# Kernel optimization log

Hardware: AMD Instinct MI355X
Metric: run time of the kernel (lower is better)

The kernel has to match this reference:

```python
import jax, jax.numpy as jnp
import numpy as np
import math

L, B, T, S, E, H, F = 6, 8, 1024, 1024, 1024, 16, 4096
HD = E // H
EPS = 1e-5

def setup_inputs() -> dict:
    key = jax.random.key(0)
    ks = jax.random.split(key, 20)
    def n(k, shape, s=0.02):
        return jax.random.normal(k, shape, dtype=jnp.float32) * s
    return {
        'encoder_output': n(ks[0], (B, S, E), 1.0),
        'decoder_input': n(ks[1], (B, T, E), 1.0),
        # LayerNorm params (stacked over layers)
        'ln1_w': jnp.ones((L, E), jnp.float32), 'ln1_b': jnp.zeros((L, E), jnp.float32),
        'ln2_w': jnp.ones((L, E), jnp.float32), 'ln2_b': jnp.zeros((L, E), jnp.float32),
        'ln3_w': jnp.ones((L, E), jnp.float32), 'ln3_b': jnp.zeros((L, E), jnp.float32),
        # self-attention: per-head wq/wk/wv concatenated into [E,E] (x @ W convention)
        'Wq_s': n(ks[2], (L, E, E)), 'Wk_s': n(ks[3], (L, E, E)), 'Wv_s': n(ks[4], (L, E, E)),
        'Wo_s': n(ks[5], (L, E, E)), 'bo_s': jnp.zeros((L, E), jnp.float32),
        # cross-attention
        'Wq_c': n(ks[6], (L, E, E)), 'Wk_c': n(ks[7], (L, E, E)), 'Wv_c': n(ks[8], (L, E, E)),
        'Wo_c': n(ks[9], (L, E, E)), 'bo_c': jnp.zeros((L, E), jnp.float32),
        # FFN
        'W1': n(ks[10], (L, E, F)), 'b1': jnp.zeros((L, F), jnp.float32),
        'W2': n(ks[11], (L, F, E)), 'b2': jnp.zeros((L, E), jnp.float32),
    }

def _layernorm(x, w, b):
    m = jnp.mean(x, axis=-1, keepdims=True)
    v = jnp.mean(jnp.square(x - m), axis=-1, keepdims=True)
    return (x - m) * jax.lax.rsqrt(v + EPS) * w + b

def _split_heads(x):
    b, s, _ = x.shape
    return x.reshape(b, s, H, HD).transpose(0, 2, 1, 3)  # [B,H,S,HD]

def _mha(q_in, k_in, v_in, Wq, Wk, Wv, Wo, bo, mask):
    q = _split_heads(q_in @ Wq)
    k = _split_heads(k_in @ Wk)
    v = _split_heads(v_in @ Wv)
    scores = jnp.einsum('bhqd,bhkd->bhqk', q, k) / math.sqrt(HD)
    if mask is not None:
        scores = jnp.where(mask, scores, jnp.float32(-jnp.inf))
    attn = jax.nn.softmax(scores, axis=-1)
    out = jnp.einsum('bhqk,bhkd->bhqd', attn, v)
    out = out.transpose(0, 2, 1, 3).reshape(q_in.shape[0], q_in.shape[1], E)
    return out @ Wo + bo

def reference(encoder_output, decoder_input,
              ln1_w, ln1_b, ln2_w, ln2_b, ln3_w, ln3_b,
              Wq_s, Wk_s, Wv_s, Wo_s, bo_s,
              Wq_c, Wk_c, Wv_c, Wo_c, bo_c,
              W1, b1, W2, b2):
    causal = jnp.tril(jnp.ones((T, T), dtype=bool))  # [T,T] -> broadcast over B,H
    params = (ln1_w, ln1_b, ln2_w, ln2_b, ln3_w, ln3_b,
              Wq_s, Wk_s, Wv_s, Wo_s, bo_s,
              Wq_c, Wk_c, Wv_c, Wo_c, bo_c,
              W1, b1, W2, b2)

    def layer(x, p):
        (l1w, l1b, l2w, l2b, l3w, l3b,
         wqs, wks, wvs, wos, bos,
         wqc, wkc, wvc, woc, boc,
         w1, bb1, w2, bb2) = p
        nx = _layernorm(x, l1w, l1b)
        x = x + _mha(nx, nx, nx, wqs, wks, wvs, wos, bos, causal)
        x = x + _mha(_layernorm(x, l2w, l2b), encoder_output, encoder_output,
                     wqc, wkc, wvc, woc, boc, None)
        h = _layernorm(x, l3w, l3b)
        x = x + (jax.nn.gelu(h @ w1 + bb1) @ w2 + bb2)
        return x, None

    out, _ = jax.lax.scan(layer, decoder_input, params)
    return out
```

## Files before the change

### kernel.cpp

```cpp
#include <hip/hip_runtime.h>
#include <cstdint>

typedef __bf16 bf16;
typedef __bf16 bf16x8 __attribute__((ext_vector_type(8)));
typedef __bf16 bf16x4 __attribute__((ext_vector_type(4)));
typedef float f32x4 __attribute__((ext_vector_type(4)));

static_assert(sizeof(bf16) == 2, "bf16 size");

constexpr int LAYERS = 6;
constexpr int BATCH  = 8;
constexpr int TDEC   = 1024;
constexpr int SENC   = 1024;
constexpr int EMB    = 1024;
constexpr int NH     = 16;
constexpr int FFN    = 4096;
constexpr int MTOK   = BATCH * TDEC;

typedef __attribute__((address_space(1))) void gvoid;
typedef __attribute__((address_space(3))) void lvoid;

__device__ __forceinline__ void gload16(const void* g, void* l) {
  __builtin_amdgcn_global_load_lds((gvoid*)(uintptr_t)g,
                                   (lvoid*)(uint32_t)(uintptr_t)l,
                                   16, 0, 0);
}

__device__ __forceinline__ f32x4 mfma_16x16x32(bf16x8 a, bf16x8 b, f32x4 c) {
  return __builtin_amdgcn_mfma_f32_16x16x32_bf16(a, b, c, 0, 0, 0);
}

__global__ void k_cvt(const float* __restrict__ in, bf16* __restrict__ outp, int n4) {
  int i = blockIdx.x * 256 + threadIdx.x;
  if (i < n4) {
    float4 v = ((const float4*)in)[i];
    bf16x4 o;
    o[0] = (bf16)v.x; o[1] = (bf16)v.y; o[2] = (bf16)v.z; o[3] = (bf16)v.w;
    ((bf16x4*)outp)[i] = o;
  }
}

__launch_bounds__(256)
__global__ void k_transpose(const float* __restrict__ in, bf16* __restrict__ outp,
                            int R, int C) {
  __shared__ float tile[32][33];
  const int tx = threadIdx.x, ty = threadIdx.y;
  const int r0 = blockIdx.y * 32, c0 = blockIdx.x * 32;
#pragma unroll
  for (int i = 0; i < 32; i += 8)
    tile[ty + i][tx] = in[(size_t)(r0 + ty + i) * C + c0 + tx];
  __syncthreads();
#pragma unroll
  for (int i = 0; i < 32; i += 8)
    outp[(size_t)(c0 + ty + i) * R + r0 + tx] = (bf16)tile[tx][ty + i];
}

__launch_bounds__(256)
__global__ void k_transpose4(const float* __restrict__ s0, const float* __restrict__ s1,
                             const float* __restrict__ s2, const float* __restrict__ s3,
                             bf16* __restrict__ d0, bf16* __restrict__ d1,
                             bf16* __restrict__ d2, bf16* __restrict__ d3,
                             int R, int C) {
  const int z = blockIdx.z;
  const float* in = (z == 0) ? s0 : (z == 1) ? s1 : (z == 2) ? s2 : s3;
  bf16* outp      = (z == 0) ? d0 : (z == 1) ? d1 : (z == 2) ? d2 : d3;
  __shared__ float tile[32][33];
  const int tx = threadIdx.x, ty = threadIdx.y;
  const int r0 = blockIdx.y * 32, c0 = blockIdx.x * 32;
#pragma unroll
  for (int i = 0; i < 32; i += 8)
    tile[ty + i][tx] = in[(size_t)(r0 + ty + i) * C + c0 + tx];
  __syncthreads();
#pragma unroll
  for (int i = 0; i < 32; i += 8)
    outp[(size_t)(c0 + ty + i) * R + r0 + tx] = (bf16)tile[tx][ty + i];
}

__launch_bounds__(256)
__global__ void k_layernorm(const float* __restrict__ x, const float* __restrict__ w,
                            const float* __restrict__ bb, bf16* __restrict__ outp) {
  const int row = blockIdx.x;
  const int t = threadIdx.x;
  const float4 v = ((const float4*)(x + (size_t)row * EMB))[t];
  float s = v.x + v.y + v.z + v.w;
  __shared__ float red[4];
#pragma unroll
  for (int off = 32; off > 0; off >>= 1) s += __shfl_down(s, off, 64);
  if ((t & 63) == 0) red[t >> 6] = s;
  __syncthreads();
  const float mean = (red[0] + red[1] + red[2] + red[3]) * (1.0f / EMB);
  const float dx = v.x - mean, dy = v.y - mean, dz = v.z - mean, dw = v.w - mean;
  float ss = dx * dx + dy * dy + dz * dz + dw * dw;
  __syncthreads();
#pragma unroll
  for (int off = 32; off > 0; off >>= 1) ss += __shfl_down(ss, off, 64);
  if ((t & 63) == 0) red[t >> 6] = ss;
  __syncthreads();
  const float var = (red[0] + red[1] + red[2] + red[3]) * (1.0f / EMB);
  const float rstd = rsqrtf(var + 1e-5f);
  const float4 wv = ((const float4*)w)[t];
  const float4 bv = ((const float4*)bb)[t];
  bf16x4 o;
  o[0] = (bf16)(dx * rstd * wv.x + bv.x);
  o[1] = (bf16)(dy * rstd * wv.y + bv.y);
  o[2] = (bf16)(dz * rstd * wv.z + bv.z);
  o[3] = (bf16)(dw * rstd * wv.w + bv.w);
  *(bf16x4*)(outp + (size_t)row * EMB + t * 4) = o;
}

template <int EPI>
__launch_bounds__(256)
__global__ void k_gemm(const bf16* __restrict__ A, const bf16* __restrict__ Bt,
                       int M, int N, int K, int ldc,
                       bf16* __restrict__ outb, float* __restrict__ outf,
                       const float* __restrict__ res, const float* __restrict__ bias) {
  __shared__ __align__(16) bf16 sA[128 * 32];
  __shared__ __align__(16) bf16 sB[128 * 32];
  const int tid = threadIdx.x;
  const int wave = tid >> 6, lane = tid & 63;
  const int quad = lane >> 4, l16 = lane & 15;
  const int wm = wave >> 1, wn = wave & 1;

  int bid = blockIdx.y * gridDim.x + blockIdx.x;
  const int nwg = gridDim.x * gridDim.y;
  if ((nwg & 7) == 0) {
    const int q = nwg >> 3;
    bid = (bid & 7) * q + (bid >> 3);
  }
  const int bn = bid % gridDim.x;
  const int bm = bid / gridDim.x;

  f32x4 acc[4][4] = {};

  const int srow = wave * 16 + (lane >> 2);
  const int scol = (lane & 3) * 8;
  const bf16* Ag = A  + (size_t)(bm * 128 + srow) * K + scol;
  const bf16* Bg = Bt + (size_t)(bn * 128 + srow) * K + scol;
  bf16* sA0 = &sA[(wave * 16) * 32];
  bf16* sA1 = &sA[(wave * 16 + 64) * 32];
  bf16* sB0 = &sB[(wave * 16) * 32];
  bf16* sB1 = &sB[(wave * 16 + 64) * 32];

  const int nk = K >> 5;
  for (int kt = 0; kt < nk; ++kt) {
    gload16(Ag, sA0);
    gload16(Ag + (size_t)64 * K, sA1);
    gload16(Bg, sB0);
    gload16(Bg + (size_t)64 * K, sB1);
    Ag += 32; Bg += 32;
    __syncthreads();
    bf16x8 af[4], bfv[4];
    const bf16* pa = &sA[(wm * 64 + l16) * 32 + quad * 8];
    const bf16* pb = &sB[(wn * 64 + l16) * 32 + quad * 8];
#pragma unroll
    for (int i = 0; i < 4; ++i) af[i] = *(const bf16x8*)(pa + i * 16 * 32);
#pragma unroll
    for (int i = 0; i < 4; ++i) bfv[i] = *(const bf16x8*)(pb + i * 16 * 32);
#pragma unroll
    for (int i = 0; i < 4; ++i)
#pragma unroll
      for (int j = 0; j < 4; ++j)
        acc[i][j] = mfma_16x16x32(af[i], bfv[j], acc[i][j]);
    __syncthreads();
  }

  const int row0 = bm * 128 + wm * 64;
  const int col0 = bn * 128 + wn * 64;
#pragma unroll
  for (int j = 0; j < 4; ++j) {
    const int c = col0 + j * 16 + l16;
    const float bv = (EPI >= 1) ? bias[c] : 0.0f;
#pragma unroll
    for (int i = 0; i < 4; ++i) {
#pragma unroll
      for (int r = 0; r < 4; ++r) {
        const size_t rr = (size_t)(row0 + i * 16 + quad * 4 + r);
        float v = acc[i][j][r];
        if (EPI == 0) {
          outb[rr * ldc + c] = (bf16)v;
        } else if (EPI == 1) {
          v += bv;
          const float u = 0.7978845608028654f * (v + 0.044715f * v * v * v);
          const float g = v / (1.0f + exp2f(u * -2.8853900817779268f));
          outb[rr * ldc + c] = (bf16)g;
        } else {
          outf[rr * ldc + c] = res[rr * ldc + c] + v + bv;
        }
      }
    }
  }
}

template <bool CAUSAL>
__launch_bounds__(256)
__global__ void k_attn(const bf16* __restrict__ Q, const bf16* __restrict__ Kg,
                       const bf16* __restrict__ Vg, bf16* __restrict__ Og,
                       int TQ, int TK, int ld) {
  __shared__ __align__(16) bf16 sK[2][64 * 64];
  __shared__ __align__(16) bf16 sVt[2][64 * 72];
  __shared__ __align__(16) bf16 sP[4][32 * 72];
  const int tid = threadIdx.x;
  const int wave = tid >> 6, lane = tid & 63;
  const int quad = lane >> 4, l16 = lane & 15;

  int bx = blockIdx.x, by = blockIdx.y;
  {
    const int nwg = gridDim.x * gridDim.y;
    if ((nwg & 7) == 0 && (gridDim.y & 7) == 0) {
      const int d = by * gridDim.x + bx;
      const int xcd = d & 7, idx = d >> 3;
      const int hpx = gridDim.y >> 3;
      by = xcd * hpx + idx / gridDim.x;
      bx = idx % gridDim.x;
    }
  }
  const int b = by >> 4;
  const int h = by & 15;
  const int qt = CAUSAL ? (gridDim.x - 1 - bx) : bx;
  const int q0 = qt * 128;
  const int qw = q0 + wave * 32;

  const bf16* Qbase = Q + (size_t)(b * TQ) * ld + h * 64;
  const bf16* Kbase = Kg + (size_t)(b * TK) * ld + h * 64;
  const bf16* Vbase = Vg + (size_t)(b * TK) * ld + h * 64;

  bf16x8 aq[2][2];
#pragma unroll
  for (int m = 0; m < 2; ++m) {
    const bf16* qp = Qbase + (size_t)(qw + m * 16 + l16) * ld + quad * 8;
    aq[m][0] = *(const bf16x8*)(qp);
    aq[m][1] = *(const bf16x8*)(qp + 32);
  }

  bf16x8 vones;
#pragma unroll
  for (int e = 0; e < 8; ++e) vones[e] = (bf16)1.0f;

  f32x4 oacc[2][4] = {};
  float m_[2][4], l_[2][4];
#pragma unroll
  for (int m = 0; m < 2; ++m)
#pragma unroll
    for (int r = 0; r < 4; ++r) { m_[m][r] = -1e30f; l_[m][r] = 0.0f; }

  const int srow = lane >> 3;
  const int schunk = lane & 7;
  bf16* sPw = &sP[wave][0];

  const float sc = 0.125f * 1.44269504088896f;
  const int nj = CAUSAL ? (q0 >> 6) + 2 : (TK >> 6);

#pragma unroll
  for (int r2 = 0; r2 < 2; ++r2) {
    const int rowt = (wave + 4 * r2) * 8 + srow;
    const int gchunk = schunk ^ (rowt & 7);
    gload16(Kbase + (size_t)rowt * ld + gchunk * 8,
            &sK[0][(wave + 4 * r2) * 8 * 64]);
  }
#pragma unroll
  for (int r2 = 0; r2 < 2; ++r2) {
    const int cv = wave + 4 * r2;
    const bf16x8 vv = *(const bf16x8*)(Vbase + (size_t)lane * ld + cv * 8);
#pragma unroll
    for (int e = 0; e < 8; ++e) sVt[0][(cv * 8 + e) * 72 + lane] = vv[e];
  }
  __syncthreads();

  int cur = 0;
  for (int j = 0; j < nj; ++j) {
    const int nxt = cur ^ 1;
    const int k0 = j * 64;
    const bool pre = (j + 1 < nj);
    bf16x8 vpre[2];
    if (pre) {
      const int k0n = k0 + 64;
#pragma unroll
      for (int r2 = 0; r2 < 2; ++r2) {
        const int rowt = (wave + 4 * r2) * 8 + srow;
        const int gchunk = schunk ^ (rowt & 7);
        gload16(Kbase + (size_t)(k0n + rowt) * ld + gchunk * 8,
                &sK[nxt][(wave + 4 * r2) * 8 * 64]);
      }
#pragma unroll
      for (int r2 = 0; r2 < 2; ++r2)
        vpre[r2] = *(const bf16x8*)(Vbase + (size_t)(k0n + lane) * ld +
                                    (wave + 4 * r2) * 8);
    }

    const bool active = !CAUSAL || (k0 <= qw + 31);
    if (active) {
#pragma unroll
      for (int m = 0; m < 2; ++m) {
        f32x4 s[4];
#pragma unroll
        for (int kt = 0; kt < 4; ++kt) {
          const int krow = kt * 16 + l16;
          const int p0 = (quad ^ (l16 & 7)) * 8;
          const int p1 = ((quad + 4) ^ (l16 & 7)) * 8;
          const bf16x8 bk0 = *(const bf16x8*)(&sK[cur][krow * 64 + p0]);
          const bf16x8 bk1 = *(const bf16x8*)(&sK[cur][krow * 64 + p1]);
          f32x4 z = {};
          z = mfma_16x16x32(aq[m][0], bk0, z);
          z = mfma_16x16x32(aq[m][1], bk1, z);
          s[kt] = z;
        }
        const int row_base = qw + m * 16;
        float rowmax[4] = {-1e30f, -1e30f, -1e30f, -1e30f};
        if (CAUSAL && (k0 + 63 > row_base)) {
#pragma unroll
          for (int kt = 0; kt < 4; ++kt) {
            const int key = k0 + kt * 16 + l16;
#pragma unroll
            for (int r = 0; r < 4; ++r) {
              if (key > row_base + quad * 4 + r) s[kt][r] = -1e30f;
              rowmax[r] = fmaxf(rowmax[r], s[kt][r]);
            }
          }
        } else {
#pragma unroll
          for (int kt = 0; kt < 4; ++kt)
#pragma unroll
            for (int r = 0; r < 4; ++r)
              rowmax[r] = fmaxf(rowmax[r], s[kt][r]);
        }
#pragma unroll
        for (int off = 1; off < 16; off <<= 1)
#pragma unroll
          for (int r = 0; r < 4; ++r)
            rowmax[r] = fmaxf(rowmax[r], __shfl_xor(rowmax[r], off, 64));
        float alpha[4], nms[4];
#pragma unroll
        for (int r = 0; r < 4; ++r) {
          const float mn = fmaxf(m_[m][r], rowmax[r]);
          alpha[r] = exp2f((m_[m][r] - mn) * sc);
          m_[m][r] = mn;
          nms[r] = -mn * sc;
        }
#pragma unroll
        for (int kt = 0; kt < 4; ++kt)
#pragma unroll
          for (int r = 0; r < 4; ++r) {
            const float pv = exp2f(fmaf(s[kt][r], sc, nms[r]));
            sPw[(m * 16 + quad * 4 + r) * 72 + kt * 16 + l16] = (bf16)pv;
          }
        const bf16x8 ap0 = *(const bf16x8*)(&sPw[(m * 16 + l16) * 72 + quad * 8]);
        const bf16x8 ap1 = *(const bf16x8*)(&sPw[(m * 16 + l16) * 72 + 32 + quad * 8]);
        f32x4 zs = {};
        zs = mfma_16x16x32(ap0, vones, zs);
        zs = mfma_16x16x32(ap1, vones, zs);
#pragma unroll
        for (int r = 0; r < 4; ++r) {
          l_[m][r] = l_[m][r] * alpha[r] + zs[r];
#pragma unroll
          for (int dt = 0; dt < 4; ++dt) oacc[m][dt][r] *= alpha[r];
        }
#pragma unroll
        for (int dt = 0; dt < 4; ++dt) {
          const bf16x8 bv0 = *(const bf16x8*)(&sVt[cur][(dt * 16 + l16) * 72 + quad * 8]);
          const bf16x8 bv1 = *(const bf16x8*)(&sVt[cur][(dt * 16 + l16) * 72 + 32 + quad * 8]);
          oacc[m][dt] = mfma_16x16x32(ap0, bv0, oacc[m][dt]);
          oacc[m][dt] = mfma_16x16x32(ap1, bv1, oacc[m][dt]);
        }
      }
    }

    if (pre) {
#pragma unroll
      for (int r2 = 0; r2 < 2; ++r2) {
        const int cv = wave + 4 * r2;
#pragma unroll
        for (int e = 0; e < 8; ++e) sVt[nxt][(cv * 8 + e) * 72 + lane] = vpre[r2][e];
      }
    }
    __syncthreads();
    cur = nxt;
  }

#pragma unroll
  for (int m = 0; m < 2; ++m)
#pragma unroll
    for (int r = 0; r < 4; ++r) {
      const float inv = 1.0f / l_[m][r];
      bf16* op = Og + (size_t)(b * TQ + qw + m * 16 + quad * 4 + r) * EMB + h * 64;
#pragma unroll
      for (int dt = 0; dt < 4; ++dt)
        op[dt * 16 + l16] = (bf16)(oacc[m][dt][r] * inv);
    }
}

extern "C" void kernel_launch(void* const* d_in, const int* in_sizes, int n_in,
                              void* d_out, int out_size, void* d_ws, size_t ws_size,
                              hipStream_t stream) {
  const float* enc  = (const float*)d_in[0];
  const float* dec  = (const float*)d_in[1];
  const float* ln1w = (const float*)d_in[2];
  const float* ln1b = (const float*)d_in[3];
  const float* ln2w = (const float*)d_in[4];
  const float* ln2b = (const float*)d_in[5];
  const float* ln3w = (const float*)d_in[6];
  const float* ln3b = (const float*)d_in[7];
  const float* Wq_s = (const float*)d_in[8];
  const float* Wk_s = (const float*)d_in[9];
  const float* Wv_s = (const float*)d_in[10];
  const float* Wo_s = (const float*)d_in[11];
  const float* bo_s = (const float*)d_in[12];
  const float* Wq_c = (const float*)d_in[13];
  const float* Wk_c = (const float*)d_in[14];
  const float* Wv_c = (const float*)d_in[15];
  const float* Wo_c = (const float*)d_in[16];
  const float* bo_c = (const float*)d_in[17];
  const float* W1   = (const float*)d_in[18];
  const float* b1   = (const float*)d_in[19];
  const float* W2   = (const float*)d_in[20];
  const float* b2   = (const float*)d_in[21];
  float* out = (float*)d_out;

  char* p = (char*)d_ws;
  auto take = [&](size_t bytes) {
    char* r = p;
    p += (bytes + 255) & ~(size_t)255;
    return (void*)r;
  };
  bf16* wqkvT = (bf16*)take((size_t)3 * EMB * EMB * 2);
  bf16* woT   = (bf16*)take((size_t)EMB * EMB * 2);
  bf16* w1T   = (bf16*)take((size_t)EMB * FFN * 2);
  bf16* w2T   = (bf16*)take((size_t)FFN * EMB * 2);
  bf16* encb  = (bf16*)take((size_t)BATCH * SENC * EMB * 2);
  float* xbuf = (float*)take((size_t)MTOK * EMB * 4);
  bf16* nx    = (bf16*)take((size_t)MTOK * EMB * 2);
  bf16* qkvb  = (bf16*)take((size_t)MTOK * 3 * EMB * 2);
  bf16* ab    = (bf16*)take((size_t)MTOK * EMB * 2);
  bf16* hb    = (bf16*)take((size_t)MTOK * FFN * 2);
  if ((size_t)((char*)p - (char*)d_ws) > ws_size) return;

  const int LD3 = 3 * EMB;

  {
    const int n4 = BATCH * SENC * EMB / 4;
    k_cvt<<<(n4 + 255) / 256, 256, 0, stream>>>(enc, encb, n4);
  }
  hipMemcpyAsync(xbuf, dec, (size_t)MTOK * EMB * 4, hipMemcpyDeviceToDevice, stream);

  auto trans = [&](const float* w, bf16* wt, int R, int C) {
    k_transpose<<<dim3(C / 32, R / 32), dim3(32, 8), 0, stream>>>(w, wt, R, C);
  };
  auto trans4 = [&](const float* s0, const float* s1, const float* s2, const float* s3,
                    bf16* d0, bf16* d1, bf16* d2, bf16* d3) {
    k_transpose4<<<dim3(EMB / 32, EMB / 32, 4), dim3(32, 8), 0, stream>>>(
        s0, s1, s2, s3, d0, d1, d2, d3, EMB, EMB);
  };
  auto gemm0 = [&](const bf16* Ap, const bf16* Btp, bf16* op, int M, int N, int K,
                   int ldc) {
    k_gemm<0><<<dim3(N / 128, M / 128), 256, 0, stream>>>(Ap, Btp, M, N, K, ldc, op,
                                                          nullptr, nullptr, nullptr);
  };
  auto gemm_gelu = [&](const bf16* Ap, const bf16* Btp, bf16* op, const float* bi,
                       int M, int N, int K) {
    k_gemm<1><<<dim3(N / 128, M / 128), 256, 0, stream>>>(Ap, Btp, M, N, K, N, op,
                                                          nullptr, nullptr, bi);
  };
  auto gemm_res = [&](const bf16* Ap, const bf16* Btp, float* op, const float* rs,
                      const float* bi, int M, int N, int K) {
    k_gemm<2><<<dim3(N / 128, M / 128), 256, 0, stream>>>(Ap, Btp, M, N, K, N, nullptr,
                                                          op, rs, bi);
  };

  for (int l = 0; l < LAYERS; ++l) {
    const size_t wofs = (size_t)l * EMB * EMB;
    k_layernorm<<<MTOK, 256, 0, stream>>>(xbuf, ln1w + l * EMB, ln1b + l * EMB, nx);
    trans4(Wq_s + wofs, Wk_s + wofs, Wv_s + wofs, Wo_s + wofs,
           wqkvT, wqkvT + (size_t)EMB * EMB, wqkvT + (size_t)2 * EMB * EMB, woT);
    gemm0(nx, wqkvT, qkvb, MTOK, 3 * EMB, EMB, LD3);
    k_attn<true><<<dim3(TDEC / 128, BATCH * NH), 256, 0, stream>>>(
        qkvb, qkvb + EMB, qkvb + 2 * EMB, ab, TDEC, TDEC, LD3);
    gemm_res(ab, woT, xbuf, xbuf, bo_s + l * EMB, MTOK, EMB, EMB);

    k_layernorm<<<MTOK, 256, 0, stream>>>(xbuf, ln2w + l * EMB, ln2b + l * EMB, nx);
    trans4(Wq_c + wofs, Wk_c + wofs, Wv_c + wofs, Wo_c + wofs,
           wqkvT, wqkvT + (size_t)EMB * EMB, wqkvT + (size_t)2 * EMB * EMB, woT);
    gemm0(nx, wqkvT, qkvb, MTOK, EMB, EMB, LD3);
    gemm0(encb, wqkvT + (size_t)EMB * EMB, qkvb + EMB, BATCH * SENC, 2 * EMB, EMB, LD3);
    k_attn<false><<<dim3(TDEC / 128, BATCH * NH), 256, 0, stream>>>(
        qkvb, qkvb + EMB, qkvb + 2 * EMB, ab, TDEC, SENC, LD3);
    gemm_res(ab, woT, xbuf, xbuf, bo_c + l * EMB, MTOK, EMB, EMB);

    k_layernorm<<<MTOK, 256, 0, stream>>>(xbuf, ln3w + l * EMB, ln3b + l * EMB, nx);
    trans(W1 + (size_t)l * EMB * FFN, w1T, EMB, FFN);
    trans(W2 + (size_t)l * FFN * EMB, w2T, FFN, EMB);
    gemm_gelu(nx, w1T, hb, b1 + (size_t)l * FFN, MTOK, FFN, EMB);
    float* fout = (l == LAYERS - 1) ? out : xbuf;
    gemm_res(hb, w2T, fout, xbuf, b2 + (size_t)l * EMB, MTOK, EMB, FFN);
  }
}
```

Before: 4.594 ms.

## Triple-buffer GEMM LDS tiles with two-stage async prefetch

The GEMM main loop now uses three LDS buffers and issues the global-to-LDS loads two k-tiles ahead. Each iteration needs only a partial vmcnt wait and a single barrier, where before it loaded, synced, computed and synced again. This is meant to hide global load latency behind the MFMA work. In exchange LDS use per block triples to 48KB, which may lower occupancy. The hand-written waitcnt must also match the compiler's actual count of outstanding vector-memory ops.

```diff
diff --git a/kernel.cpp b/kernel.cpp
--- a/kernel.cpp
+++ b/kernel.cpp
@@ -114,8 +114,8 @@
                        int M, int N, int K, int ldc,
                        bf16* __restrict__ outb, float* __restrict__ outf,
                        const float* __restrict__ res, const float* __restrict__ bias) {
-  __shared__ __align__(16) bf16 sA[128 * 32];
-  __shared__ __align__(16) bf16 sB[128 * 32];
+  __shared__ __align__(16) bf16 sA[3][128 * 32];
+  __shared__ __align__(16) bf16 sB[3][128 * 32];
   const int tid = threadIdx.x;
   const int wave = tid >> 6, lane = tid & 63;
   const int quad = lane >> 4, l16 = lane & 15;
@@ -136,22 +136,34 @@
   const int scol = (lane & 3) * 8;
   const bf16* Ag = A  + (size_t)(bm * 128 + srow) * K + scol;
   const bf16* Bg = Bt + (size_t)(bn * 128 + srow) * K + scol;
-  bf16* sA0 = &sA[(wave * 16) * 32];
-  bf16* sA1 = &sA[(wave * 16 + 64) * 32];
-  bf16* sB0 = &sB[(wave * 16) * 32];
-  bf16* sB1 = &sB[(wave * 16 + 64) * 32];
+
+  auto stage = [&](int buf, int kt) {
+    const bf16* ag = Ag + kt * 32;
+    const bf16* bg = Bg + kt * 32;
+    gload16(ag,                  &sA[buf][(wave * 16) * 32]);
+    gload16(ag + (size_t)64 * K, &sA[buf][(wave * 16 + 64) * 32]);
+    gload16(bg,                  &sB[buf][(wave * 16) * 32]);
+    gload16(bg + (size_t)64 * K, &sB[buf][(wave * 16 + 64) * 32]);
+  };
 
   const int nk = K >> 5;
+  stage(0, 0);
+  if (nk > 1) {
+    stage(1, 1);
+    asm volatile("s_waitcnt vmcnt(4)" ::: "memory");
+  } else {
+    asm volatile("s_waitcnt vmcnt(0)" ::: "memory");
+  }
+  __builtin_amdgcn_s_barrier();
+
+  int cur = 0;
   for (int kt = 0; kt < nk; ++kt) {
-    gload16(Ag, sA0);
-    gload16(Ag + (size_t)64 * K, sA1);
-    gload16(Bg, sB0);
-    gload16(Bg + (size_t)64 * K, sB1);
-    Ag += 32; Bg += 32;
-    __syncthreads();
+    int nxt2 = cur + 2; if (nxt2 >= 3) nxt2 -= 3;
+    if (kt + 2 < nk) stage(nxt2, kt + 2);
+
     bf16x8 af[4], bfv[4];
-    const bf16* pa = &sA[(wm * 64 + l16) * 32 + quad * 8];
-    const bf16* pb = &sB[(wn * 64 + l16) * 32 + quad * 8];
+    const bf16* pa = &sA[cur][(wm * 64 + l16) * 32 + quad * 8];
+    const bf16* pb = &sB[cur][(wn * 64 + l16) * 32 + quad * 8];
 #pragma unroll
     for (int i = 0; i < 4; ++i) af[i] = *(const bf16x8*)(pa + i * 16 * 32);
 #pragma unroll
@@ -161,7 +173,15 @@
 #pragma unroll
       for (int j = 0; j < 4; ++j)
         acc[i][j] = mfma_16x16x32(af[i], bfv[j], acc[i][j]);
-    __syncthreads();
+
+    if (kt + 2 < nk) {
+      asm volatile("s_waitcnt vmcnt(4)" ::: "memory");
+      __builtin_amdgcn_s_barrier();
+    } else if (kt + 1 < nk) {
+      asm volatile("s_waitcnt vmcnt(0)" ::: "memory");
+      __builtin_amdgcn_s_barrier();
+    }
+    cur = (cur + 1 == 3) ? 0 : cur + 1;
   }
 
   const int row0 = bm * 128 + wm * 64;
```

Measured after the change: 4.227 ms. 1.09x faster.
